# Kernel optimization log

Hardware: AMD Instinct MI355X
Metric: run time of the kernel (lower is better)

The kernel has to match this reference:

```python
import jax, jax.numpy as jnp
import numpy as np

B, T, D_MODEL, N_HEADS = 2, 2048, 2048, 16
HEAD_DIM = D_MODEL // N_HEADS
SCALE = HEAD_DIM ** -0.5
ROPE_THETA = 10000.0


def setup_inputs() -> dict:
    key = jax.random.key(0)
    ks = jax.random.split(key, 5)
    std = D_MODEL ** -0.5
    return {
        "x": jax.random.normal(ks[0], (B, T, D_MODEL), dtype=jnp.float32),
        "Wq": jax.random.normal(ks[1], (D_MODEL, D_MODEL), dtype=jnp.float32) * std,
        "Wk": jax.random.normal(ks[2], (D_MODEL, D_MODEL), dtype=jnp.float32) * std,
        "Wv": jax.random.normal(ks[3], (D_MODEL, D_MODEL), dtype=jnp.float32) * std,
        "Wo": jax.random.normal(ks[4], (D_MODEL, D_MODEL), dtype=jnp.float32) * std,
    }


def _rope_cos_sin(t, dtype):
    inv_freq = 1.0 / (ROPE_THETA ** (jnp.arange(0, HEAD_DIM, 2, dtype=jnp.float32) / HEAD_DIM))
    freqs = jnp.arange(t, dtype=jnp.float32)[:, None] * inv_freq[None, :]  # (T, hd/2)
    emb = jnp.concatenate([freqs, freqs], axis=-1)  # (T, hd)
    return jnp.cos(emb).astype(dtype), jnp.sin(emb).astype(dtype)


def _rotate_half(x):
    x1, x2 = jnp.split(x, 2, axis=-1)
    return jnp.concatenate([-x2, x1], axis=-1)


def _apply_rope(q, k):
    # q, k: (B, H, T, hd)
    cos, sin = _rope_cos_sin(q.shape[2], q.dtype)
    cos = cos[None, None]  # (1,1,T,hd)
    sin = sin[None, None]
    q = q * cos + _rotate_half(q) * sin
    k = k * cos + _rotate_half(k) * sin
    return q, k


def reference(x, Wq, Wk, Wv, Wo):
    b, t, _ = x.shape
    # projections (nn.Linear: x @ W.T), split heads: b t (h d) -> b h t d
    def proj(W):
        return jnp.einsum('btm,nm->btn', x, W).reshape(b, t, N_HEADS, HEAD_DIM).transpose(0, 2, 1, 3)
    Q, K, V = proj(Wq), proj(Wk), proj(Wv)
    Q, K = _apply_rope(Q, K)
    scores = jnp.einsum('bhtd,bhsd->bhts', Q, K) * SCALE  # (B,H,T,T)
    causal_mask = jnp.tril(jnp.ones((t, t), dtype=bool))
    scores = jnp.where(causal_mask[None, None], scores, -jnp.inf)
    attn = jax.nn.softmax(scores, axis=-1)
    attn = jnp.nan_to_num(attn, nan=0.0)
    out = jnp.einsum('bhts,bhsd->bhtd', attn, V)
    out = out.transpose(0, 2, 1, 3).reshape(b, t, D_MODEL)
    return jnp.einsum('btm,nm->btn', out, Wo)
```

## Files before the change

kernel.cpp:

```cpp
#include <hip/hip_runtime.h>

typedef unsigned short ushort_t;
typedef short bf16x8 __attribute__((ext_vector_type(8)));
typedef float f32x4 __attribute__((ext_vector_type(4)));

#define D_MODEL 2048
#define T_SEQ 2048
#define NB 2
#define NH 16
#define HD 128
#define M_ROWS 4096

__device__ __forceinline__ float b2f(unsigned short u) {
    return __uint_as_float(((unsigned)u) << 16);
}
__device__ __forceinline__ unsigned short f2b(float f) {
    unsigned u = __float_as_uint(f);
    u += 0x7fffu + ((u >> 16) & 1u);
    return (unsigned short)(u >> 16);
}

__device__ __forceinline__ void g2l16(const ushort_t* g, ushort_t* l) {
    __builtin_amdgcn_global_load_lds(
        (const __attribute__((address_space(1))) unsigned int*)g,
        (__attribute__((address_space(3))) unsigned int*)l, 16, 0, 0);
}

__global__ void detect_dtype(const ushort_t* __restrict__ x, int* __restrict__ flag) {
    __shared__ int cnt;
    if (threadIdx.x == 0) cnt = 0;
    __syncthreads();
    int c = 0;
    for (int i = threadIdx.x; i < 8192; i += 256) {
        int e = (x[i] >> 7) & 0xFF;
        if (e >= 0xC8) ++c;
    }
    atomicAdd(&cnt, c);
    __syncthreads();
    if (threadIdx.x == 0) *flag = (cnt > 16) ? 1 : 0;
}

#define NCONVB 12288
#define NROPEB 512

__global__ void convert_rope(const void* __restrict__ s0, const void* __restrict__ s1,
                             const void* __restrict__ s2, const void* __restrict__ s3,
                             const void* __restrict__ s4, ushort_t* __restrict__ dst,
                             float* __restrict__ rtab,
                             int hostfl, const int* __restrict__ flag) {
    const int bx = blockIdx.x;
    if (bx >= NCONVB) {
        int tid = (bx - NCONVB) * 256 + threadIdx.x;
        int i = tid & 63, t = tid >> 6;
        float ang = (float)t * exp2f(-(float)i * 0.20762050593046015f);
        rtab[t * 128 + i]      = cosf(ang);
        rtab[t * 128 + 64 + i] = sinf(ang);
        return;
    }
    const size_t TENc = (size_t)M_ROWS * D_MODEL;
    const size_t WELc = (size_t)D_MODEL * D_MODEL;
    size_t i = ((size_t)bx * 256 + threadIdx.x) * 8;
    const void* src;
    size_t off;
    if (i < TENc) {
        src = s0; off = i;
    } else {
        size_t j = i - TENc;
        int wsel = (int)(j >> 22);
        src = (wsel == 0) ? s1 : (wsel == 1) ? s2 : (wsel == 2) ? s3 : s4;
        off = j & (WELc - 1);
    }
    const int fl = (hostfl >= 0) ? hostfl : *flag;
    if (fl) {
        const float* s = (const float*)src + off;
        union { ushort_t u[8]; float4 f; } pk;
        #pragma unroll
        for (int j2 = 0; j2 < 8; ++j2) pk.u[j2] = f2b(s[j2]);
        *(float4*)(dst + i) = pk.f;
    } else {
        *(float4*)(dst + i) = *(const float4*)((const ushort_t*)src + off);
    }
}

#define ABUF3 (256 * 32)
#define WBUF3 (128 * 32)
#define PBUF3 (ABUF3 + WBUF3)

__device__ __forceinline__ void gemm3_body(const ushort_t* __restrict__ A,
                                           const ushort_t* __restrict__ W,
                                           ushort_t* __restrict__ C,
                                           float* __restrict__ outf,
                                           int fl,
                                           const float* __restrict__ rtab,
                                           int mode, int Ndim,
                                           long bm, long bn,
                                           ushort_t* smem) {
    const int tid  = threadIdx.x;
    const int lane = tid & 63;
    const int w    = tid >> 6;
    const int wr   = w >> 1;
    const int wc   = w & 1;
    const int quad = lane >> 4, l16 = lane & 15;
    const int Kd   = D_MODEL;

    f32x4 acc[4][4];
    #pragma unroll
    for (int i = 0; i < 4; ++i)
        #pragma unroll
        for (int j = 0; j < 4; ++j) acc[i][j] = {0.f, 0.f, 0.f, 0.f};

    const int lr = lane >> 2;
    const int cl = lane & 3;
    const int rowA0 = (w * 2 + 0) * 16 + lr;
    const int rowA1 = (w * 2 + 1) * 16 + lr;
    const int rowW  = w * 16 + lr;
    const ushort_t* gA0 = A + (bm + rowA0) * Kd + ((cl ^ ((rowA0 >> 1) & 3)) * 8);
    const ushort_t* gA1 = A + (bm + rowA1) * Kd + ((cl ^ ((rowA1 >> 1) & 3)) * 8);
    const ushort_t* gW  = W + (bn + rowW)  * Kd + ((cl ^ ((rowW  >> 1) & 3)) * 8);

    const int fsl = (l16 >> 1) & 3;

    auto stage = [&](int s, int sb) {
        ushort_t* As = smem + sb * PBUF3;
        ushort_t* Ws = As + ABUF3;
        const int ko = s * 32;
        g2l16(gA0 + ko, As + (w * 2 + 0) * 512);
        g2l16(gA1 + ko, As + (w * 2 + 1) * 512);
        g2l16(gW + ko, Ws + w * 512);
    };

    auto kstep = [&](int s, int rb, int vm, bool do_stage) {
        if (vm == 3) asm volatile("s_waitcnt vmcnt(3)" ::: "memory");
        else         asm volatile("s_waitcnt vmcnt(0)" ::: "memory");
        __builtin_amdgcn_sched_barrier(0);
        __builtin_amdgcn_s_barrier();
        __builtin_amdgcn_sched_barrier(0);
        if (do_stage) stage(s + 2, (rb + 2) % 3);
        const ushort_t* As = smem + rb * PBUF3;
        const ushort_t* Ws = As + ABUF3;
        bf16x8 af[4], bf[4];
        #pragma unroll
        for (int i = 0; i < 4; ++i)
            af[i] = *(const bf16x8*)(As + (wr * 64 + i * 16 + l16) * 32 + (quad ^ fsl) * 8);
        #pragma unroll
        for (int j = 0; j < 4; ++j)
            bf[j] = *(const bf16x8*)(Ws + (wc * 64 + j * 16 + l16) * 32 + (quad ^ fsl) * 8);
        __builtin_amdgcn_s_setprio(1);
        #pragma unroll
        for (int i = 0; i < 4; ++i)
            #pragma unroll
            for (int j = 0; j < 4; ++j)
                acc[i][j] = __builtin_amdgcn_mfma_f32_16x16x32_bf16(af[i], bf[j], acc[i][j], 0, 0, 0);
        __builtin_amdgcn_s_setprio(0);
    };

    stage(0, 0); stage(1, 1);
    for (int s = 0; s < 60; s += 3) {
        kstep(s + 0, 0, 3, true);
        kstep(s + 1, 1, 3, true);
        kstep(s + 2, 2, 3, true);
    }
    kstep(60, 0, 3, true);
    kstep(61, 1, 3, true);
    kstep(62, 2, 3, false);
    kstep(63, 0, 0, false);
    __syncthreads();

    if (mode == 2) {
        #pragma unroll
        for (int i = 0; i < 4; ++i)
            #pragma unroll
            for (int j = 0; j < 4; ++j)
                #pragma unroll
                for (int r = 0; r < 4; ++r) {
                    int row = wr * 64 + i * 16 + quad * 4 + r;
                    int col = wc * 64 + j * 16 + l16;
                    smem[col * 256 + ((((row >> 3) ^ (col & 7)) << 3) | (row & 7))] =
                        f2b(acc[i][j][r]);
                }
        __syncthreads();
        const int b = (int)(bm >> 11), t0 = (int)(bm & 2047), h = (int)(bn >> 7);
        const size_t obase = ((size_t)(b * NH + h) * HD) * T_SEQ;
        #pragma unroll
        for (int it = 0; it < 8; ++it) {
            int dd  = it * 16 + (tid >> 5);
            int tch = tid & 31;
            bf16x8 v = *(const bf16x8*)(smem + dd * 256 + ((tch ^ (dd & 7)) << 3));
            *(bf16x8*)(C + obase + (size_t)dd * T_SEQ + t0 + tch * 8) = v;
        }
        return;
    }

    const int as_f32 = (outf != nullptr) && (fl != 0);
    if (!as_f32) {
        #pragma unroll
        for (int i = 0; i < 4; ++i)
            #pragma unroll
            for (int j = 0; j < 4; ++j)
                #pragma unroll
                for (int r = 0; r < 4; ++r) {
                    int row = wr * 64 + i * 16 + quad * 4 + r;
                    int col = wc * 64 + j * 16 + l16;
                    int ch = col >> 3, off = col & 7;
                    smem[row * 128 + (((ch ^ (row & 7)) << 3) | off)] = f2b(acc[i][j][r]);
                }
        __syncthreads();
        if (mode == 1) {
            #pragma unroll
            for (int it = 0; it < 8; ++it) {
                int row = it * 32 + (tid >> 4);
                int ch  = tid & 15;
                int t = (int)((bm + row) & 2047);
                bf16x8 v = *(const bf16x8*)(smem + row * 128 + ((ch ^ (row & 7)) << 3));
                bf16x8 p = *(const bf16x8*)(smem + row * 128 + (((ch ^ 8) ^ (row & 7)) << 3));
                const float* cr = rtab + t * 128 + (ch & 7) * 8;
                float sgn = (ch < 8) ? -1.f : 1.f;
                union { ushort_t u[8]; float4 f[1]; } o;
                #pragma unroll
                for (int j = 0; j < 8; ++j) {
                    float cv = cr[j], sv = cr[64 + j];
                    o.u[j] = f2b(b2f(((const ushort_t*)&v)[j]) * cv +
                                 sgn * b2f(((const ushort_t*)&p)[j]) * sv);
                }
                *(bf16x8*)(C + (bm + row) * Ndim + bn + ch * 8) = *(const bf16x8*)o.u;
            }
        } else {
            #pragma unroll
            for (int it = 0; it < 8; ++it) {
                int row = it * 32 + (tid >> 4);
                int ch  = tid & 15;
                bf16x8 v = *(const bf16x8*)(smem + row * 128 + ((ch ^ (row & 7)) << 3));
                *(bf16x8*)(C + (bm + row) * Ndim + bn + ch * 8) = v;
            }
        }
    } else {
        float* Fs = (float*)smem;
        #pragma unroll
        for (int half = 0; half < 2; ++half) {
            __syncthreads();
            if ((wr >> 1) == half) {
                #pragma unroll
                for (int i = 0; i < 4; ++i)
                    #pragma unroll
                    for (int j = 0; j < 4; ++j)
                        #pragma unroll
                        for (int r = 0; r < 4; ++r) {
                            int lrow = (wr & 1) * 64 + i * 16 + quad * 4 + r;
                            int col = wc * 64 + j * 16 + l16;
                            int ch = col >> 2, off = col & 3;
                            Fs[lrow * 128 + (((ch ^ (lrow & 7)) << 2) | off)] = acc[i][j][r];
                        }
            }
            __syncthreads();
            #pragma unroll
            for (int it = 0; it < 8; ++it) {
                int lrow = it * 16 + (tid >> 5);
                int ch = tid & 31;
                float4 v = *(const float4*)(Fs + lrow * 128 + ((ch ^ (lrow & 7)) << 2));
                *(float4*)(outf + (bm + half * 128 + lrow) * Ndim + bn + ch * 4) = v;
            }
        }
    }
}

__global__ __launch_bounds__(512) void gemm_qkv3(const ushort_t* __restrict__ A,
                                                 const ushort_t* __restrict__ Wq,
                                                 const ushort_t* __restrict__ Wk,
                                                 const ushort_t* __restrict__ Wv,
                                                 ushort_t* __restrict__ Qo,
                                                 ushort_t* __restrict__ Ko,
                                                 ushort_t* __restrict__ Vto,
                                                 const float* __restrict__ rtab) {
    __shared__ ushort_t smem[3 * PBUF3];
    const int wsel = blockIdx.y >> 4;
    const int ym   = blockIdx.y & 15;
    const ushort_t* W = (wsel == 0) ? Wq : (wsel == 1) ? Wk : Wv;
    ushort_t* C       = (wsel == 0) ? Qo : (wsel == 1) ? Ko : Vto;
    const int mode = (wsel == 2) ? 2 : 1;
    const int wg  = ym * 16 + blockIdx.x;
    const int swz = (wg & 7) * 32 + (wg >> 3);
    const long bm = (long)(swz >> 4) * 256;
    const long bn = (long)(swz & 15) * 128;
    gemm3_body(A, W, C, nullptr, 0, rtab, mode, D_MODEL, bm, bn, smem);
}

__global__ __launch_bounds__(512) void gemm_nt3(const ushort_t* __restrict__ A,
                                                const ushort_t* __restrict__ W,
                                                ushort_t* __restrict__ C,
                                                float* __restrict__ outf,
                                                int hostfl,
                                                const int* __restrict__ flag,
                                                const float* __restrict__ rtab,
                                                int mode, int Ndim) {
    __shared__ ushort_t smem[3 * PBUF3];
    const int wg  = blockIdx.y * 16 + blockIdx.x;
    const int swz = (wg & 7) * 32 + (wg >> 3);
    const long bm = (long)(swz >> 4) * 256;
    const long bn = (long)(swz & 15) * 128;
    int fl = (hostfl >= 0) ? hostfl : *flag;
    asm volatile("" :: "v"(fl));
    asm volatile("s_waitcnt vmcnt(0)" ::: "memory");
    gemm3_body(A, W, C, outf, fl, rtab, mode, Ndim, bm, bn, smem);
}

#define NQT (T_SEQ / 64)
#define C2SM 0.1275174452f
#define MFIX 96.0f

__global__ __launch_bounds__(256, 4) void attn_kernel(const ushort_t* __restrict__ Q,
                                                      const ushort_t* __restrict__ K,
                                                      const ushort_t* __restrict__ Vt,
                                                      ushort_t* __restrict__ O) {
    __shared__ ushort_t Ks[64 * 128];
    __shared__ ushort_t Vs[128 * 64];
    __shared__ ushort_t Ps[4 * 16 * 64];

    const int tid = threadIdx.x;
    const int lane = tid & 63, w = tid >> 6;
    const int quad = lane >> 4, l16 = lane & 15;
    const int bx = blockIdx.x;
    const int g = bx >> 5;
    int qb;
    if (g < 8)       qb = 31 - g;
    else if (g < 16) qb = g - 8;
    else if (g < 24) qb = 39 - g;
    else             qb = g - 16;
    const int bh = bx & 31;
    const int h = bh & 15, b = bh >> 4;

    const size_t qkbase = ((size_t)(b * T_SEQ)) * D_MODEL + h * HD;
    const size_t vtbase = ((size_t)((b * NH + h) * HD)) * T_SEQ;
    const int ck0 = w * 256 + lane;
    ushort_t* Pw = Ps + w * 1024;

    auto stage_K = [&](int kvb) {
        #pragma unroll
        for (int i = 0; i < 4; ++i) {
            int ck = ck0 + i * 64;
            int r = ck >> 4, gg = (ck & 15) ^ (r & 15);
            g2l16(K + qkbase + (size_t)(kvb * 64 + r) * D_MODEL + gg * 8,
                  (ushort_t*)Ks + (size_t)(w * 256 + i * 64) * 8);
        }
    };
    auto stage_V = [&](int kvb) {
        #pragma unroll
        for (int i = 0; i < 4; ++i) {
            int ck = ck0 + i * 64;
            int r = ck >> 3, gg = (ck & 7) ^ (r & 7);
            g2l16(Vt + vtbase + (size_t)r * T_SEQ + kvb * 64 + gg * 8,
                  (ushort_t*)Vs + (size_t)(w * 256 + i * 64) * 8);
        }
    };

    bf16x8 qf[4];
    {
        const ushort_t* qrow = Q + qkbase + (size_t)(qb * 64 + w * 16 + l16) * D_MODEL;
        #pragma unroll
        for (int ks = 0; ks < 4; ++ks)
            qf[ks] = *(const bf16x8*)(qrow + ks * 32 + quad * 8);
    }

    float l_i[4] = {0.f, 0.f, 0.f, 0.f};
    f32x4 accO[8];
    for (int i = 0; i < 8; ++i) accO[i] = {0.f, 0.f, 0.f, 0.f};

    stage_K(0);

    for (int kvb = 0; kvb <= qb; ++kvb) {
        __syncthreads();
        stage_V(kvb);

        f32x4 accS[4];
        for (int i = 0; i < 4; ++i) accS[i] = {0.f, 0.f, 0.f, 0.f};
        __builtin_amdgcn_s_setprio(1);
        #pragma unroll
        for (int ks = 0; ks < 4; ++ks) {
            #pragma unroll
            for (int ct = 0; ct < 4; ++ct) {
                bf16x8 bb = *(const bf16x8*)(Ks + (ct * 16 + l16) * 128 +
                                             (((ks * 4 + quad) ^ l16) * 8));
                accS[ct] = __builtin_amdgcn_mfma_f32_16x16x32_bf16(qf[ks], bb, accS[ct], 0, 0, 0);
            }
        }
        __builtin_amdgcn_s_setprio(0);

        if (kvb == qb) {
            int qloc = w * 16 + quad * 4;
            for (int ct = 0; ct < 4; ++ct) {
                int key = ct * 16 + l16;
                for (int r = 0; r < 4; ++r)
                    if (key > qloc + r) accS[ct][r] = -1e30f;
            }
        }

        #pragma unroll
        for (int ct = 0; ct < 4; ++ct) {
            #pragma unroll
            for (int r = 0; r < 4; ++r) {
                float pv = exp2f((accS[ct][r] - MFIX) * C2SM);
                l_i[r] += pv;
                int col = ct * 16 + l16;
                int row = quad * 4 + r;
                Pw[row * 64 + ((((col >> 3) ^ (row & 7)) << 3) | (col & 7))] = f2b(pv);
            }
        }

        __syncthreads();
        if (kvb < qb) stage_K(kvb + 1);

        __builtin_amdgcn_s_setprio(1);
        #pragma unroll
        for (int kk2 = 0; kk2 < 2; ++kk2) {
            bf16x8 a = *(const bf16x8*)(Pw + l16 * 64 + (((kk2 * 4 + quad) ^ (l16 & 7)) << 3));
            #pragma unroll
            for (int ct = 0; ct < 8; ++ct) {
                bf16x8 bb = *(const bf16x8*)(Vs + (ct * 16 + l16) * 64 +
                                             (((kk2 * 4 + quad) ^ (l16 & 7)) * 8));
                accO[ct] = __builtin_amdgcn_mfma_f32_16x16x32_bf16(a, bb, accO[ct], 0, 0, 0);
            }
        }
        __builtin_amdgcn_s_setprio(0);
    }

    #pragma unroll
    for (int r = 0; r < 4; ++r) {
        for (int off = 1; off < 16; off <<= 1)
            l_i[r] += __shfl_xor(l_i[r], off);
        l_i[r] = 1.f / l_i[r];
    }

    for (int ct = 0; ct < 8; ++ct)
        for (int r = 0; r < 4; ++r) {
            size_t row = (size_t)(b * T_SEQ + qb * 64 + w * 16 + quad * 4 + r);
            O[row * D_MODEL + h * HD + ct * 16 + l16] = f2b(accO[ct][r] * l_i[r]);
        }
}

extern "C" void kernel_launch(void* const* d_in, const int* in_sizes, int n_in,
                              void* d_out, int out_size, void* d_ws, size_t ws_size,
                              hipStream_t stream) {
    const size_t TEN = (size_t)M_ROWS * D_MODEL;
    const size_t WEL = (size_t)D_MODEL * D_MODEL;

    char* ws = (char*)d_ws;
    int* flag = (int*)ws;
    ushort_t* xb  = (ushort_t*)(ws + 256);
    ushort_t* Wqb = xb  + TEN;
    ushort_t* Wkb = Wqb + WEL;
    ushort_t* Wvb = Wkb + WEL;
    ushort_t* Wob = Wvb + WEL;
    ushort_t* Qb  = Wob + WEL;
    ushort_t* Kb  = Qb + TEN;
    ushort_t* attn = Kb + TEN;
    ushort_t* Vt  = attn + TEN;
    float* rtab = (float*)(Vt + TEN);

    int hostfl = -1;
    if (in_sizes && n_in > 0) {
        if (in_sizes[0] == (int)(TEN * 4)) hostfl = 1;
        else if (in_sizes[0] == (int)(TEN * 2)) hostfl = 0;
    }
    if (hostfl < 0)
        detect_dtype<<<1, 256, 0, stream>>>((const ushort_t*)d_in[0], flag);

    convert_rope<<<NCONVB + NROPEB, 256, 0, stream>>>(
        d_in[0], d_in[1], d_in[2], d_in[3], d_in[4], xb, rtab, hostfl, flag);

    gemm_qkv3<<<dim3(16, 48), 512, 0, stream>>>(xb, Wqb, Wkb, Wvb, Qb, Kb, Vt, rtab);

    attn_kernel<<<dim3(NQT * NB * NH), 256, 0, stream>>>(Qb, Kb, Vt, attn);

    gemm_nt3<<<dim3(16, 16), 512, 0, stream>>>(attn, Wob, (ushort_t*)d_out,
                                               (float*)d_out, hostfl, flag, rtab,
                                               0, D_MODEL);
}
```

Baseline: 372.0 us.

## Halve GEMM block to 4 warps with 128x64 per-warp tiles

Changes the projection GEMMs from 8 waves per block with 64x64 warp tiles to 4 waves per block with 128x64 warp tiles, keeping the 256x128 block tile. Each wave now issues more global-to-LDS loads per stage, and the vmcnt wait is adjusted to match. The intent is more MFMA work per LDS fragment load and less barrier overhead per unit of work. In exchange, register pressure per wave doubles (32 accumulators), which may limit occupancy, and fewer waves are available to hide latency.

```diff
diff --git a/kernel.cpp b/kernel.cpp
--- a/kernel.cpp
+++ b/kernel.cpp
@@ -82,11 +82,11 @@
     }
 }
 
-#define ABUF3 (256 * 32)
-#define WBUF3 (128 * 32)
-#define PBUF3 (ABUF3 + WBUF3)
-
-__device__ __forceinline__ void gemm3_body(const ushort_t* __restrict__ A,
+#define ABUF4 (256 * 32)
+#define WBUF4 (128 * 32)
+#define PBUF4 (ABUF4 + WBUF4)
+
+__device__ __forceinline__ void gemm4_body(const ushort_t* __restrict__ A,
                                            const ushort_t* __restrict__ W,
                                            ushort_t* __restrict__ C,
                                            float* __restrict__ outf,
@@ -98,56 +98,55 @@
     const int tid  = threadIdx.x;
     const int lane = tid & 63;
     const int w    = tid >> 6;
-    const int wr   = w >> 1;
-    const int wc   = w & 1;
+    const int wrg  = w >> 1;
+    const int wcg  = w & 1;
     const int quad = lane >> 4, l16 = lane & 15;
-    const int Kd   = D_MODEL;
-
-    f32x4 acc[4][4];
+
+    f32x4 acc[8][4];
     #pragma unroll
-    for (int i = 0; i < 4; ++i)
+    for (int i = 0; i < 8; ++i)
         #pragma unroll
         for (int j = 0; j < 4; ++j) acc[i][j] = {0.f, 0.f, 0.f, 0.f};
 
     const int lr = lane >> 2;
     const int cl = lane & 3;
-    const int rowA0 = (w * 2 + 0) * 16 + lr;
-    const int rowA1 = (w * 2 + 1) * 16 + lr;
-    const int rowW  = w * 16 + lr;
-    const ushort_t* gA0 = A + (bm + rowA0) * Kd + ((cl ^ ((rowA0 >> 1) & 3)) * 8);
-    const ushort_t* gA1 = A + (bm + rowA1) * Kd + ((cl ^ ((rowA1 >> 1) & 3)) * 8);
-    const ushort_t* gW  = W + (bn + rowW)  * Kd + ((cl ^ ((rowW  >> 1) & 3)) * 8);
+    const int csw = cl ^ ((lr >> 1) & 3);
+    const ushort_t* gA = A + (bm + w * 64 + lr) * D_MODEL + csw * 8;
+    const ushort_t* gW = W + (bn + w * 32 + lr) * D_MODEL + csw * 8;
 
     const int fsl = (l16 >> 1) & 3;
 
     auto stage = [&](int s, int sb) {
-        ushort_t* As = smem + sb * PBUF3;
-        ushort_t* Ws = As + ABUF3;
+        ushort_t* As = smem + sb * PBUF4;
+        ushort_t* Ws = As + ABUF4;
         const int ko = s * 32;
-        g2l16(gA0 + ko, As + (w * 2 + 0) * 512);
-        g2l16(gA1 + ko, As + (w * 2 + 1) * 512);
-        g2l16(gW + ko, Ws + w * 512);
+        #pragma unroll
+        for (int i = 0; i < 4; ++i)
+            g2l16(gA + i * 16 * D_MODEL + ko, As + (w * 4 + i) * 512);
+        #pragma unroll
+        for (int i = 0; i < 2; ++i)
+            g2l16(gW + i * 16 * D_MODEL + ko, Ws + (w * 2 + i) * 512);
     };
 
     auto kstep = [&](int s, int rb, int vm, bool do_stage) {
-        if (vm == 3) asm volatile("s_waitcnt vmcnt(3)" ::: "memory");
+        if (vm == 6) asm volatile("s_waitcnt vmcnt(6)" ::: "memory");
         else         asm volatile("s_waitcnt vmcnt(0)" ::: "memory");
         __builtin_amdgcn_sched_barrier(0);
         __builtin_amdgcn_s_barrier();
         __builtin_amdgcn_sched_barrier(0);
         if (do_stage) stage(s + 2, (rb + 2) % 3);
-        const ushort_t* As = smem + rb * PBUF3;
-        const ushort_t* Ws = As + ABUF3;
-        bf16x8 af[4], bf[4];
-        #pragma unroll
-        for (int i = 0; i < 4; ++i)
-            af[i] = *(const bf16x8*)(As + (wr * 64 + i * 16 + l16) * 32 + (quad ^ fsl) * 8);
+        const ushort_t* As = smem + rb * PBUF4;
+        const ushort_t* Ws = As + ABUF4;
+        bf16x8 af[8], bf[4];
+        #pragma unroll
+        for (int i = 0; i < 8; ++i)
+            af[i] = *(const bf16x8*)(As + (wrg * 128 + i * 16 + l16) * 32 + (quad ^ fsl) * 8);
         #pragma unroll
         for (int j = 0; j < 4; ++j)
-            bf[j] = *(const bf16x8*)(Ws + (wc * 64 + j * 16 + l16) * 32 + (quad ^ fsl) * 8);
+            bf[j] = *(const bf16x8*)(Ws + (wcg * 64 + j * 16 + l16) * 32 + (quad ^ fsl) * 8);
         __builtin_amdgcn_s_setprio(1);
         #pragma unroll
-        for (int i = 0; i < 4; ++i)
+        for (int i = 0; i < 8; ++i)
             #pragma unroll
             for (int j = 0; j < 4; ++j)
                 acc[i][j] = __builtin_amdgcn_mfma_f32_16x16x32_bf16(af[i], bf[j], acc[i][j], 0, 0, 0);
@@ -156,25 +155,25 @@
 
     stage(0, 0); stage(1, 1);
     for (int s = 0; s < 60; s += 3) {
-        kstep(s + 0, 0, 3, true);
-        kstep(s + 1, 1, 3, true);
-        kstep(s + 2, 2, 3, true);
-    }
-    kstep(60, 0, 3, true);
-    kstep(61, 1, 3, true);
-    kstep(62, 2, 3, false);
+        kstep(s + 0, 0, 6, true);
+        kstep(s + 1, 1, 6, true);
+        kstep(s + 2, 2, 6, true);
+    }
+    kstep(60, 0, 6, true);
+    kstep(61, 1, 6, true);
+    kstep(62, 2, 6, false);
     kstep(63, 0, 0, false);
     __syncthreads();
 
     if (mode == 2) {
         #pragma unroll
-        for (int i = 0; i < 4; ++i)
+        for (int i = 0; i < 8; ++i)
             #pragma unroll
             for (int j = 0; j < 4; ++j)
                 #pragma unroll
                 for (int r = 0; r < 4; ++r) {
-                    int row = wr * 64 + i * 16 + quad * 4 + r;
-                    int col = wc * 64 + j * 16 + l16;
+                    int row = wrg * 128 + i * 16 + quad * 4 + r;
+                    int col = wcg * 64 + j * 16 + l16;
                     smem[col * 256 + ((((row >> 3) ^ (col & 7)) << 3) | (row & 7))] =
                         f2b(acc[i][j][r]);
                 }
@@ -182,8 +181,8 @@
         const int b = (int)(bm >> 11), t0 = (int)(bm & 2047), h = (int)(bn >> 7);
         const size_t obase = ((size_t)(b * NH + h) * HD) * T_SEQ;
         #pragma unroll
-        for (int it = 0; it < 8; ++it) {
-            int dd  = it * 16 + (tid >> 5);
+        for (int it = 0; it < 16; ++it) {
+            int dd  = it * 8 + (tid >> 5);
             int tch = tid & 31;
             bf16x8 v = *(const bf16x8*)(smem + dd * 256 + ((tch ^ (dd & 7)) << 3));
             *(bf16x8*)(C + obase + (size_t)dd * T_SEQ + t0 + tch * 8) = v;
@@ -194,21 +193,21 @@
     const int as_f32 = (outf != nullptr) && (fl != 0);
     if (!as_f32) {
         #pragma unroll
-        for (int i = 0; i < 4; ++i)
+        for (int i = 0; i < 8; ++i)
             #pragma unroll
             for (int j = 0; j < 4; ++j)
                 #pragma unroll
                 for (int r = 0; r < 4; ++r) {
-                    int row = wr * 64 + i * 16 + quad * 4 + r;
-                    int col = wc * 64 + j * 16 + l16;
+                    int row = wrg * 128 + i * 16 + quad * 4 + r;
+                    int col = wcg * 64 + j * 16 + l16;
                     int ch = col >> 3, off = col & 7;
                     smem[row * 128 + (((ch ^ (row & 7)) << 3) | off)] = f2b(acc[i][j][r]);
                 }
         __syncthreads();
         if (mode == 1) {
             #pragma unroll
-            for (int it = 0; it < 8; ++it) {
-                int row = it * 32 + (tid >> 4);
+            for (int it = 0; it < 16; ++it) {
+                int row = it * 16 + (tid >> 4);
                 int ch  = tid & 15;
                 int t = (int)((bm + row) & 2047);
                 bf16x8 v = *(const bf16x8*)(smem + row * 128 + ((ch ^ (row & 7)) << 3));
@@ -226,8 +225,8 @@
             }
         } else {
             #pragma unroll
-            for (int it = 0; it < 8; ++it) {
-                int row = it * 32 + (tid >> 4);
+            for (int it = 0; it < 16; ++it) {
+                int row = it * 16 + (tid >> 4);
                 int ch  = tid & 15;
                 bf16x8 v = *(const bf16x8*)(smem + row * 128 + ((ch ^ (row & 7)) << 3));
                 *(bf16x8*)(C + (bm + row) * Ndim + bn + ch * 8) = v;
@@ -238,23 +237,23 @@
         #pragma unroll
         for (int half = 0; half < 2; ++half) {
             __syncthreads();
-            if ((wr >> 1) == half) {
+            if (wrg == half) {
                 #pragma unroll
-                for (int i = 0; i < 4; ++i)
+                for (int i = 0; i < 8; ++i)
                     #pragma unroll
                     for (int j = 0; j < 4; ++j)
                         #pragma unroll
                         for (int r = 0; r < 4; ++r) {
-                            int lrow = (wr & 1) * 64 + i * 16 + quad * 4 + r;
-                            int col = wc * 64 + j * 16 + l16;
+                            int lrow = i * 16 + quad * 4 + r;
+                            int col = wcg * 64 + j * 16 + l16;
                             int ch = col >> 2, off = col & 3;
                             Fs[lrow * 128 + (((ch ^ (lrow & 7)) << 2) | off)] = acc[i][j][r];
                         }
             }
             __syncthreads();
             #pragma unroll
-            for (int it = 0; it < 8; ++it) {
-                int lrow = it * 16 + (tid >> 5);
+            for (int it = 0; it < 16; ++it) {
+                int lrow = it * 8 + (tid >> 5);
                 int ch = tid & 31;
                 float4 v = *(const float4*)(Fs + lrow * 128 + ((ch ^ (lrow & 7)) << 2));
                 *(float4*)(outf + (bm + half * 128 + lrow) * Ndim + bn + ch * 4) = v;
@@ -263,15 +262,15 @@
     }
 }
 
-__global__ __launch_bounds__(512) void gemm_qkv3(const ushort_t* __restrict__ A,
-                                                 const ushort_t* __restrict__ Wq,
-                                                 const ushort_t* __restrict__ Wk,
-                                                 const ushort_t* __restrict__ Wv,
-                                                 ushort_t* __restrict__ Qo,
-                                                 ushort_t* __restrict__ Ko,
-                                                 ushort_t* __restrict__ Vto,
-                                                 const float* __restrict__ rtab) {
-    __shared__ ushort_t smem[3 * PBUF3];
+__global__ __launch_bounds__(256, 2) void gemm_qkv3(const ushort_t* __restrict__ A,
+                                                    const ushort_t* __restrict__ Wq,
+                                                    const ushort_t* __restrict__ Wk,
+                                                    const ushort_t* __restrict__ Wv,
+                                                    ushort_t* __restrict__ Qo,
+                                                    ushort_t* __restrict__ Ko,
+                                                    ushort_t* __restrict__ Vto,
+                                                    const float* __restrict__ rtab) {
+    __shared__ ushort_t smem[3 * PBUF4];
     const int wsel = blockIdx.y >> 4;
     const int ym   = blockIdx.y & 15;
     const ushort_t* W = (wsel == 0) ? Wq : (wsel == 1) ? Wk : Wv;
@@ -281,18 +280,18 @@
     const int swz = (wg & 7) * 32 + (wg >> 3);
     const long bm = (long)(swz >> 4) * 256;
     const long bn = (long)(swz & 15) * 128;
-    gemm3_body(A, W, C, nullptr, 0, rtab, mode, D_MODEL, bm, bn, smem);
-}
-
-__global__ __launch_bounds__(512) void gemm_nt3(const ushort_t* __restrict__ A,
-                                                const ushort_t* __restrict__ W,
-                                                ushort_t* __restrict__ C,
-                                                float* __restrict__ outf,
-                                                int hostfl,
-                                                const int* __restrict__ flag,
-                                                const float* __restrict__ rtab,
-                                                int mode, int Ndim) {
-    __shared__ ushort_t smem[3 * PBUF3];
+    gemm4_body(A, W, C, nullptr, 0, rtab, mode, D_MODEL, bm, bn, smem);
+}
+
+__global__ __launch_bounds__(256, 2) void gemm_nt3(const ushort_t* __restrict__ A,
+                                                   const ushort_t* __restrict__ W,
+                                                   ushort_t* __restrict__ C,
+                                                   float* __restrict__ outf,
+                                                   int hostfl,
+                                                   const int* __restrict__ flag,
+                                                   const float* __restrict__ rtab,
+                                                   int mode, int Ndim) {
+    __shared__ ushort_t smem[3 * PBUF4];
     const int wg  = blockIdx.y * 16 + blockIdx.x;
     const int swz = (wg & 7) * 32 + (wg >> 3);
     const long bm = (long)(swz >> 4) * 256;
@@ -300,7 +299,7 @@
     int fl = (hostfl >= 0) ? hostfl : *flag;
     asm volatile("" :: "v"(fl));
     asm volatile("s_waitcnt vmcnt(0)" ::: "memory");
-    gemm3_body(A, W, C, outf, fl, rtab, mode, Ndim, bm, bn, smem);
+    gemm4_body(A, W, C, outf, fl, rtab, mode, Ndim, bm, bn, smem);
 }
 
 #define NQT (T_SEQ / 64)
@@ -466,11 +465,11 @@
     convert_rope<<<NCONVB + NROPEB, 256, 0, stream>>>(
         d_in[0], d_in[1], d_in[2], d_in[3], d_in[4], xb, rtab, hostfl, flag);
 
-    gemm_qkv3<<<dim3(16, 48), 512, 0, stream>>>(xb, Wqb, Wkb, Wvb, Qb, Kb, Vt, rtab);
+    gemm_qkv3<<<dim3(16, 48), 256, 0, stream>>>(xb, Wqb, Wkb, Wvb, Qb, Kb, Vt, rtab);
 
     attn_kernel<<<dim3(NQT * NB * NH), 256, 0, stream>>>(Qb, Kb, Vt, attn);
 
-    gemm_nt3<<<dim3(16, 16), 512, 0, stream>>>(attn, Wob, (ushort_t*)d_out,
+    gemm_nt3<<<dim3(16, 16), 256, 0, stream>>>(attn, Wob, (ushort_t*)d_out,
                                                (float*)d_out, hostfl, flag, rtab,
                                                0, D_MODEL);
 }
```

New measurement: 372.5 us. About the same (+0.1%).

## Deepen GEMM pipeline to four LDS stages with register double-buffered fragments

Applied to the files above, without the earlier changes.

The GEMM main loop moves from a 3-stage to a 4-stage shared-memory ring and double-buffers the MFMA operand fragments in registers. The next k-step's LDS fragment loads are issued before the current step's MFMAs, so LDS read latency is meant to overlap with matrix math, and global prefetch runs one stage further ahead. In exchange it uses more shared memory and more VGPRs, which could lower occupancy. The loop schedule and wait counts are restructured to match.

```diff
diff --git a/kernel.cpp b/kernel.cpp
--- a/kernel.cpp
+++ b/kernel.cpp
@@ -129,41 +129,58 @@
         g2l16(gW + ko, Ws + w * 512);
     };
 
-    auto kstep = [&](int s, int rb, int vm, bool do_stage) {
-        if (vm == 3) asm volatile("s_waitcnt vmcnt(3)" ::: "memory");
-        else         asm volatile("s_waitcnt vmcnt(0)" ::: "memory");
+    bf16x8 afA[4], bfA[4], afB[4], bfB[4];
+
+    auto ldfrags = [&](int rb, bf16x8 (&af)[4], bf16x8 (&bf)[4]) {
+        const ushort_t* As = smem + rb * PBUF3;
+        const ushort_t* Ws = As + ABUF3;
+        #pragma unroll
+        for (int i = 0; i < 4; ++i)
+            af[i] = *(const bf16x8*)(As + (wr * 64 + i * 16 + l16) * 32 + (quad ^ fsl) * 8);
+        #pragma unroll
+        for (int j = 0; j < 4; ++j)
+            bf[j] = *(const bf16x8*)(Ws + (wc * 64 + j * 16 + l16) * 32 + (quad ^ fsl) * 8);
+    };
+
+    auto domfma = [&](bf16x8 (&af)[4], bf16x8 (&bf)[4]) {
+        __builtin_amdgcn_s_setprio(1);
+        #pragma unroll
+        for (int i = 0; i < 4; ++i)
+            #pragma unroll
+            for (int j = 0; j < 4; ++j)
+                acc[i][j] = __builtin_amdgcn_mfma_f32_16x16x32_bf16(af[i], bf[j], acc[i][j], 0, 0, 0);
+        __builtin_amdgcn_s_setprio(0);
+    };
+
+    auto step = [&](int s, int rbn, bf16x8 (&cA)[4], bf16x8 (&cB)[4],
+                    bf16x8 (&nA)[4], bf16x8 (&nB)[4], int vm, bool stg, bool ld) {
+        if (vm == 3)      asm volatile("s_waitcnt vmcnt(3)" ::: "memory");
+        else if (vm == 0) asm volatile("s_waitcnt vmcnt(0)" ::: "memory");
         __builtin_amdgcn_sched_barrier(0);
         __builtin_amdgcn_s_barrier();
         __builtin_amdgcn_sched_barrier(0);
-        if (do_stage) stage(s + 2, (rb + 2) % 3);
-        const ushort_t* As = smem + rb * PBUF3;
-        const ushort_t* Ws = As + ABUF3;
-        bf16x8 af[4], bf[4];
-        #pragma unroll
-        for (int i = 0; i < 4; ++i)
-            af[i] = *(const bf16x8*)(As + (wr * 64 + i * 16 + l16) * 32 + (quad ^ fsl) * 8);
-        #pragma unroll
-        for (int j = 0; j < 4; ++j)
-            bf[j] = *(const bf16x8*)(Ws + (wc * 64 + j * 16 + l16) * 32 + (quad ^ fsl) * 8);
-        __builtin_amdgcn_s_setprio(1);
-        #pragma unroll
-        for (int i = 0; i < 4; ++i)
-            #pragma unroll
-            for (int j = 0; j < 4; ++j)
-                acc[i][j] = __builtin_amdgcn_mfma_f32_16x16x32_bf16(af[i], bf[j], acc[i][j], 0, 0, 0);
-        __builtin_amdgcn_s_setprio(0);
-    };
-
-    stage(0, 0); stage(1, 1);
-    for (int s = 0; s < 60; s += 3) {
-        kstep(s + 0, 0, 3, true);
-        kstep(s + 1, 1, 3, true);
-        kstep(s + 2, 2, 3, true);
-    }
-    kstep(60, 0, 3, true);
-    kstep(61, 1, 3, true);
-    kstep(62, 2, 3, false);
-    kstep(63, 0, 0, false);
+        if (stg) stage(s + 3, (s + 3) & 3);
+        if (ld) ldfrags(rbn, nA, nB);
+        domfma(cA, cB);
+    };
+
+    stage(0, 0); stage(1, 1); stage(2, 2);
+    asm volatile("s_waitcnt vmcnt(6)" ::: "memory");
+    __builtin_amdgcn_sched_barrier(0);
+    __builtin_amdgcn_s_barrier();
+    __builtin_amdgcn_sched_barrier(0);
+    ldfrags(0, afA, bfA);
+
+    for (int s4 = 0; s4 < 60; s4 += 4) {
+        step(s4 + 0, (s4 + 1) & 3, afA, bfA, afB, bfB, 3, true, true);
+        step(s4 + 1, (s4 + 2) & 3, afB, bfB, afA, bfA, 3, true, true);
+        step(s4 + 2, (s4 + 3) & 3, afA, bfA, afB, bfB, 3, true, true);
+        step(s4 + 3, (s4 + 4) & 3, afB, bfB, afA, bfA, 3, true, true);
+    }
+    step(60, 61 & 3, afA, bfA, afB, bfB, 3, true, true);
+    step(61, 62 & 3, afB, bfB, afA, bfA, 3, false, true);
+    step(62, 63 & 3, afA, bfA, afB, bfB, 0, false, true);
+    step(63, 0,      afB, bfB, afA, bfA, -1, false, false);
     __syncthreads();
 
     if (mode == 2) {
@@ -271,7 +288,7 @@
                                                  ushort_t* __restrict__ Ko,
                                                  ushort_t* __restrict__ Vto,
                                                  const float* __restrict__ rtab) {
-    __shared__ ushort_t smem[3 * PBUF3];
+    __shared__ ushort_t smem[4 * PBUF3];
     const int wsel = blockIdx.y >> 4;
     const int ym   = blockIdx.y & 15;
     const ushort_t* W = (wsel == 0) ? Wq : (wsel == 1) ? Wk : Wv;
@@ -292,7 +309,7 @@
                                                 const int* __restrict__ flag,
                                                 const float* __restrict__ rtab,
                                                 int mode, int Ndim) {
-    __shared__ ushort_t smem[3 * PBUF3];
+    __shared__ ushort_t smem[4 * PBUF3];
     const int wg  = blockIdx.y * 16 + blockIdx.x;
     const int swz = (wg & 7) * 32 + (wg >> 3);
     const long bm = (long)(swz >> 4) * 256;
```

After: 371.8 us. No clear change (-0.1%).
